# Optimization experiments

Measured on AMD Instinct MI355X. Metric: run time of the kernel, lower is better.

## Reference

```python
import jax, jax.numpy as jnp
import numpy as np

NUM_USERS = 1_000_000
NUM_AGES = 8
NUM_ATTR = 40
FACE_K = 64
VISUAL_DIM = 2048
HIDDEN = 512
BATCH = 16384
VOCAB = NUM_USERS + 24 + 2 + NUM_AGES + NUM_ATTR  # fm_linear input width


def setup_inputs() -> dict:
    key = jax.random.key(0)
    ks = jax.random.split(key, 24)
    s = 0.02
    inp = {
        "user_id": jax.random.randint(ks[0], (BATCH,), 0, NUM_USERS),
        "hour": jax.random.randint(ks[1], (BATCH,), 0, 24),
        "visual": jax.random.normal(ks[2], (BATCH, VISUAL_DIM), jnp.float32),
        "scale": jax.random.uniform(ks[3], (BATCH, 1), jnp.float32),
        "gender": jax.random.randint(ks[4], (BATCH,), 0, 2),
        "age": jax.random.randint(ks[5], (BATCH,), 0, NUM_AGES),
        "attribute": jax.random.randint(ks[6], (BATCH,), 0, NUM_ATTR),
        # embedding tables
        "user_emb": jax.random.normal(ks[7], (NUM_USERS, FACE_K), jnp.float32) * s,
        "hour_emb": jax.random.normal(ks[8], (24, FACE_K), jnp.float32) * s,
        "gender_emb": jax.random.normal(ks[9], (2, FACE_K), jnp.float32) * s,
        "age_emb": jax.random.normal(ks[10], (NUM_AGES, FACE_K), jnp.float32) * s,
        "attr_emb": jax.random.normal(ks[11], (NUM_ATTR, FACE_K), jnp.float32) * s,
        # visual linear
        "visu_w": jax.random.normal(ks[12], (FACE_K, VISUAL_DIM), jnp.float32) * s,
        "visu_b": jnp.zeros((FACE_K,), jnp.float32),
        # fm linear over concatenated one-hots (width VOCAB, out 2)
        "fm_w": jax.random.normal(ks[13], (2, VOCAB), jnp.float32) * s,
        "fm_b": jnp.zeros((2,), jnp.float32),
        # dnn
        "w1": jax.random.normal(ks[14], (HIDDEN, 6 * FACE_K), jnp.float32) * s,
        "b1": jnp.zeros((HIDDEN,), jnp.float32),
        "w2": jax.random.normal(ks[15], (HIDDEN, HIDDEN), jnp.float32) * s,
        "b2": jnp.zeros((HIDDEN,), jnp.float32),
        "w3": jax.random.normal(ks[16], (2, HIDDEN), jnp.float32) * s,
        "b3": jnp.zeros((2,), jnp.float32),
    }
    return inp


def reference(user_id, hour, visual, scale, gender, age, attribute,
              user_emb, hour_emb, gender_emb, age_emb, attr_emb,
              visu_w, visu_b, fm_w, fm_b, w1, b1, w2, b2, w3, b3):
    B = user_id.shape[0]
    # fm linear: one_hot @ W^T == gather-sum of W columns at the hot indices
    cols = jnp.stack([
        user_id,
        NUM_USERS + hour,
        NUM_USERS + 24 + gender,
        NUM_USERS + 24 + 2 + age,
        NUM_USERS + 24 + 2 + NUM_AGES + attribute,
    ], axis=1)  # [B, 5]
    linear_part = fm_w[:, cols].sum(axis=2).T + fm_b  # [B, 2]

    # embeddings
    user = user_emb[user_id]            # [B, K]
    hr = hour_emb[hour]                 # [B, K]
    face = jnp.stack([gender_emb[gender], attr_emb[attribute], age_emb[age]], axis=1)  # [B,3,K]
    face = scale[:, None, :] * jnp.tanh(face)  # scale [B,1] -> [B,1,1]
    embeddings = jnp.concatenate([user[:, None, :], hr[:, None, :], face], axis=1)  # [B,5,K]

    # FM second order
    so = jnp.square(embeddings.sum(axis=1)) - jnp.square(embeddings).sum(axis=1)  # [B,K]
    second_order = 0.5 * so.sum(axis=1)  # [B]
    fm = linear_part + second_order[:, None]  # [B,2]

    # DNN
    vis = visual @ visu_w.T + visu_b  # [B,K]
    x = jnp.concatenate([embeddings.reshape(B, 5 * FACE_K), vis], axis=1)  # [B,6K]
    x = jax.nn.relu(x @ w1.T + b1)
    x = jax.nn.relu(x @ w2.T + b2)
    x = x @ w3.T + b3
    return jax.nn.softmax(fm + x, axis=1)
```

## Files before the change

### kernel.cpp

```cpp
#include <hip/hip_runtime.h>
#include <hip/hip_bf16.h>
#include <stdint.h>

#define BATCH 16384
#define FACE_K 64
#define VISUAL_DIM 2048
#define HIDDEN 512
#define NUM_USERS 1000000
#define NUM_AGES 8
#define NUM_ATTR 40
#define VOCAB (NUM_USERS + 24 + 2 + NUM_AGES + NUM_ATTR)
#define XDIM 384
#define LDS_S 516

typedef __bf16 bf16x8 __attribute__((ext_vector_type(8)));
typedef float f32x4 __attribute__((ext_vector_type(4)));

__device__ __forceinline__ uint16_t f2bf(float f) {
    union { float f; uint32_t u; } v; v.f = f;
    uint32_t r = v.u + 0x7fffu + ((v.u >> 16) & 1u);
    return (uint16_t)(r >> 16);
}
__device__ __forceinline__ float bf2f(uint16_t h) {
    union { uint32_t u; float f; } v; v.u = ((uint32_t)h) << 16;
    return v.f;
}

__global__ void cvt_all(const float* __restrict__ visu_w, const float* __restrict__ w1,
                        const float* __restrict__ w2, uint16_t* __restrict__ vwb,
                        uint16_t* __restrict__ w1b, uint16_t* __restrict__ w2b) {
    int i = blockIdx.x * blockDim.x + threadIdx.x;
    const float4* src;
    ushort4* dst;
    if (i < 32768)       { src = (const float4*)visu_w + i;        dst = (ushort4*)vwb + i; }
    else if (i < 81920)  { src = (const float4*)w1 + (i - 32768);  dst = (ushort4*)w1b + (i - 32768); }
    else                 { src = (const float4*)w2 + (i - 81920);  dst = (ushort4*)w2b + (i - 81920); }
    float4 v = *src;
    ushort4 o;
    o.x = f2bf(v.x); o.y = f2bf(v.y); o.z = f2bf(v.z); o.w = f2bf(v.w);
    *dst = o;
}

#define VIS_BLOCKS 1024
__global__ __launch_bounds__(256) void front_kernel(
        const float* __restrict__ visual, const uint16_t* __restrict__ Wb,
        const float* __restrict__ bias,
        const int* __restrict__ uid, const int* __restrict__ hour,
        const float* __restrict__ scale, const int* __restrict__ gender,
        const int* __restrict__ age, const int* __restrict__ attr,
        const float* __restrict__ user_emb, const float* __restrict__ hour_emb,
        const float* __restrict__ gender_emb, const float* __restrict__ age_emb,
        const float* __restrict__ attr_emb,
        const float* __restrict__ fm_w, const float* __restrict__ fm_b,
        uint16_t* __restrict__ x, float* __restrict__ fm) {
    __shared__ float red[3 * 64 * 17];
    int t = threadIdx.x;
    int wv = t >> 6, lane = t & 63;

    if (blockIdx.x < VIS_BLOCKS) {
        int lc = lane & 15, quad = lane >> 4;
        int m0 = blockIdx.x * 16;
        const float*    ap = visual + (size_t)(m0 + lc) * VISUAL_DIM + wv * 512 + quad * 8;
        const uint16_t* wp = Wb + (size_t)lc * VISUAL_DIM + wv * 512 + quad * 8;

        f32x4 acc[4];
        #pragma unroll
        for (int j = 0; j < 4; ++j) acc[j] = (f32x4){0.f, 0.f, 0.f, 0.f};

        #pragma unroll 4
        for (int k = 0; k < 512; k += 32) {
            float4 a0 = *(const float4*)(ap + k);
            float4 a1 = *(const float4*)(ap + k + 4);
            bf16x8 af;
            af[0] = (__bf16)a0.x; af[1] = (__bf16)a0.y; af[2] = (__bf16)a0.z; af[3] = (__bf16)a0.w;
            af[4] = (__bf16)a1.x; af[5] = (__bf16)a1.y; af[6] = (__bf16)a1.z; af[7] = (__bf16)a1.w;
            #pragma unroll
            for (int j = 0; j < 4; ++j) {
                bf16x8 bf = *(const bf16x8*)(wp + (size_t)(j * 16) * VISUAL_DIM + k);
                acc[j] = __builtin_amdgcn_mfma_f32_16x16x32_bf16(af, bf, acc[j], 0, 0, 0);
            }
        }
        if (wv) {
            int base = (wv - 1) * 1088 + lane * 17;
            #pragma unroll
            for (int j = 0; j < 4; ++j)
                #pragma unroll
                for (int r = 0; r < 4; ++r)
                    red[base + j * 4 + r] = acc[j][r];
        }
        __syncthreads();
        if (wv == 0) {
            int base = lane * 17;
            #pragma unroll
            for (int j = 0; j < 4; ++j) {
                int col = j * 16 + lc;
                float b = bias[col];
                #pragma unroll
                for (int r = 0; r < 4; ++r) {
                    float sum = acc[j][r] + red[base + j * 4 + r]
                              + red[1088 + base + j * 4 + r] + red[2176 + base + j * 4 + r];
                    int row = m0 + quad * 4 + r;
                    x[(size_t)row * XDIM + 320 + col] = f2bf(sum + b);
                }
            }
        }
    } else {
        int row = (blockIdx.x - VIS_BLOCKS) * 4 + wv;
        int u = uid[row], h = hour[row], g = gender[row], a = age[row], at = attr[row];
        float sc = scale[row];
        float eu  = user_emb[(size_t)u * 64 + lane];
        float eh  = hour_emb[h * 64 + lane];
        float eg  = sc * tanhf(gender_emb[g * 64 + lane]);
        float eat = sc * tanhf(attr_emb[at * 64 + lane]);
        float eag = sc * tanhf(age_emb[a * 64 + lane]);
        float s  = eu + eh + eg + eat + eag;
        float sq = eu*eu + eh*eh + eg*eg + eat*eat + eag*eag;
        float so = s * s - sq;
        float l0 = 0.f, l1 = 0.f;
        if (lane < 5) {
            int col = (lane == 0) ? u
                    : (lane == 1) ? (NUM_USERS + h)
                    : (lane == 2) ? (NUM_USERS + 24 + g)
                    : (lane == 3) ? (NUM_USERS + 26 + a)
                    :               (NUM_USERS + 34 + at);
            l0 = fm_w[col];
            l1 = fm_w[VOCAB + col];
        }
        for (int m = 32; m; m >>= 1) {
            so += __shfl_xor(so, m);
            l0 += __shfl_xor(l0, m);
            l1 += __shfl_xor(l1, m);
        }
        if (lane == 0) {
            fm[row * 2 + 0] = l0 + fm_b[0] + 0.5f * so;
            fm[row * 2 + 1] = l1 + fm_b[1] + 0.5f * so;
        }
        size_t xb = (size_t)row * XDIM;
        x[xb +       lane] = f2bf(eu);
        x[xb +  64 + lane] = f2bf(eh);
        x[xb + 128 + lane] = f2bf(eg);
        x[xb + 192 + lane] = f2bf(eat);
        x[xb + 256 + lane] = f2bf(eag);
    }
}

__global__ __launch_bounds__(256) void fused_dnn(
        const uint16_t* __restrict__ x, const uint16_t* __restrict__ w1b,
        const float* __restrict__ b1, const uint16_t* __restrict__ w2b,
        const float* __restrict__ b2, const float* __restrict__ w3,
        const float* __restrict__ b3, const float* __restrict__ fm,
        float* __restrict__ out) {
    __shared__ uint16_t h1s[32 * LDS_S];
    __shared__ float dred[2][16][2];
    int t = threadIdx.x;
    int wv = t >> 6, lane = t & 63;
    int rg = wv >> 1, cs = wv & 1;
    int lc = lane & 15, quad = lane >> 4;
    int m0 = blockIdx.x * 32 + rg * 16;

    const uint16_t* ap  = x + (size_t)(m0 + lc) * XDIM + quad * 8;
    const uint16_t* wp1 = w1b + (size_t)(cs * 256 + lc) * XDIM + quad * 8;

    f32x4 acc[16];
    #pragma unroll
    for (int j = 0; j < 16; ++j) acc[j] = (f32x4){0.f, 0.f, 0.f, 0.f};

    #pragma unroll 2
    for (int ks = 0; ks < 12; ++ks) {
        bf16x8 af = *(const bf16x8*)(ap + ks * 32);
        #pragma unroll
        for (int j = 0; j < 16; ++j) {
            bf16x8 bf = *(const bf16x8*)(wp1 + (size_t)(j * 16) * XDIM + ks * 32);
            acc[j] = __builtin_amdgcn_mfma_f32_16x16x32_bf16(af, bf, acc[j], 0, 0, 0);
        }
    }
    #pragma unroll
    for (int j = 0; j < 16; ++j) {
        int col = cs * 256 + j * 16 + lc;
        float bb = b1[col];
        #pragma unroll
        for (int r = 0; r < 4; ++r) {
            float v = fmaxf(acc[j][r] + bb, 0.f);
            h1s[(rg * 16 + quad * 4 + r) * LDS_S + col] = f2bf(v);
        }
    }
    __syncthreads();

    const uint16_t* lp  = h1s + (rg * 16 + lc) * LDS_S + quad * 8;
    const uint16_t* wp2 = w2b + (size_t)(cs * 256 + lc) * HIDDEN + quad * 8;

    f32x4 acc2[16];
    #pragma unroll
    for (int j = 0; j < 16; ++j) acc2[j] = (f32x4){0.f, 0.f, 0.f, 0.f};

    #pragma unroll 2
    for (int ks = 0; ks < 16; ++ks) {
        union { bf16x8 v; ushort4 h[2]; } u;
        u.h[0] = *(const ushort4*)(lp + ks * 32);
        u.h[1] = *(const ushort4*)(lp + ks * 32 + 4);
        bf16x8 af = u.v;
        #pragma unroll
        for (int j = 0; j < 16; ++j) {
            bf16x8 bf = *(const bf16x8*)(wp2 + (size_t)(j * 16) * HIDDEN + ks * 32);
            acc2[j] = __builtin_amdgcn_mfma_f32_16x16x32_bf16(af, bf, acc2[j], 0, 0, 0);
        }
    }

    float d0[4] = {0.f, 0.f, 0.f, 0.f}, d1[4] = {0.f, 0.f, 0.f, 0.f};
    #pragma unroll
    for (int j = 0; j < 16; ++j) {
        int col = cs * 256 + j * 16 + lc;
        float bb = b2[col];
        float wa = w3[col], wb2v = w3[HIDDEN + col];
        #pragma unroll
        for (int r = 0; r < 4; ++r) {
            float v = fmaxf(acc2[j][r] + bb, 0.f);
            d0[r] += v * wa;
            d1[r] += v * wb2v;
        }
    }
    #pragma unroll
    for (int m = 1; m <= 8; m <<= 1) {
        #pragma unroll
        for (int r = 0; r < 4; ++r) {
            d0[r] += __shfl_xor(d0[r], m);
            d1[r] += __shfl_xor(d1[r], m);
        }
    }
    if (cs == 1 && lc == 0) {
        #pragma unroll
        for (int r = 0; r < 4; ++r) {
            dred[rg][quad * 4 + r][0] = d0[r];
            dred[rg][quad * 4 + r][1] = d1[r];
        }
    }
    __syncthreads();
    if (cs == 0 && lc == 0) {
        #pragma unroll
        for (int r = 0; r < 4; ++r) {
            int row = m0 + quad * 4 + r;
            float l0 = fm[row * 2 + 0] + d0[r] + dred[rg][quad * 4 + r][0] + b3[0];
            float l1 = fm[row * 2 + 1] + d1[r] + dred[rg][quad * 4 + r][1] + b3[1];
            float mx = fmaxf(l0, l1);
            float e0 = __expf(l0 - mx), e1 = __expf(l1 - mx);
            float inv = 1.f / (e0 + e1);
            out[row * 2 + 0] = e0 * inv;
            out[row * 2 + 1] = e1 * inv;
        }
    }
}

extern "C" void kernel_launch(void* const* d_in, const int* in_sizes, int n_in,
                              void* d_out, int out_size, void* d_ws, size_t ws_size,
                              hipStream_t stream) {
    const int*   user_id   = (const int*)d_in[0];
    const int*   hour      = (const int*)d_in[1];
    const float* visual    = (const float*)d_in[2];
    const float* scale     = (const float*)d_in[3];
    const int*   gender    = (const int*)d_in[4];
    const int*   age       = (const int*)d_in[5];
    const int*   attribute = (const int*)d_in[6];
    const float* user_emb  = (const float*)d_in[7];
    const float* hour_emb  = (const float*)d_in[8];
    const float* gender_emb= (const float*)d_in[9];
    const float* age_emb   = (const float*)d_in[10];
    const float* attr_emb  = (const float*)d_in[11];
    const float* visu_w    = (const float*)d_in[12];
    const float* visu_b    = (const float*)d_in[13];
    const float* fm_w      = (const float*)d_in[14];
    const float* fm_b      = (const float*)d_in[15];
    const float* w1        = (const float*)d_in[16];
    const float* b1        = (const float*)d_in[17];
    const float* w2        = (const float*)d_in[18];
    const float* b2        = (const float*)d_in[19];
    const float* w3        = (const float*)d_in[20];
    const float* b3        = (const float*)d_in[21];
    float* out = (float*)d_out;

    char* ws = (char*)d_ws;
    uint16_t* x   = (uint16_t*)ws;
    float*    fm  = (float*)   (ws + 12582912);
    uint16_t* vwb = (uint16_t*)(ws + 12582912 + 131072);
    uint16_t* w1b = vwb + 64 * 2048;
    uint16_t* w2b = w1b + 512 * 384;

    cvt_all<<<576, 256, 0, stream>>>(visu_w, w1, w2, vwb, w1b, w2b);
    front_kernel<<<VIS_BLOCKS + BATCH / 4, 256, 0, stream>>>(
        visual, vwb, visu_b,
        user_id, hour, scale, gender, age, attribute,
        user_emb, hour_emb, gender_emb, age_emb, attr_emb,
        fm_w, fm_b, x, fm);
    fused_dnn<<<BATCH / 32, 256, 0, stream>>>(x, w1b, b1, w2b, b2, w3, b3, fm, out);
}
```

Baseline: 534.1 us.

## Fuse front embedding/visual stage and DNN into one per-tile mega kernel

Merges the embedding/FM stage, the visual projection and the two-layer DNN into a single kernel where each 32-row block builds its x tile in LDS instead of writing x and fm to global memory and reading them back. The DNN GEMMs now have each wave cover 128 columns for both 16-row groups, so every weight fragment load feeds two MFMAs. This removes a kernel launch and the global round trip of the intermediate activations. In exchange the grid shrinks to 512 blocks, each running a long serial chain of phases, which lowers parallelism and latency hiding for the visual load (the dominant byte stream), and LDS use per block rises.

```diff
diff --git a/kernel.cpp b/kernel.cpp
--- a/kernel.cpp
+++ b/kernel.cpp
@@ -11,7 +11,8 @@
 #define NUM_ATTR 40
 #define VOCAB (NUM_USERS + 24 + 2 + NUM_AGES + NUM_ATTR)
 #define XDIM 384
-#define LDS_S 516
+#define XS 388
+#define HS 516
 
 typedef __bf16 bf16x8 __attribute__((ext_vector_type(8)));
 typedef float f32x4 __attribute__((ext_vector_type(4)));
@@ -20,10 +21,6 @@
     union { float f; uint32_t u; } v; v.f = f;
     uint32_t r = v.u + 0x7fffu + ((v.u >> 16) & 1u);
     return (uint16_t)(r >> 16);
-}
-__device__ __forceinline__ float bf2f(uint16_t h) {
-    union { uint32_t u; float f; } v; v.u = ((uint32_t)h) << 16;
-    return v.f;
 }
 
 __global__ void cvt_all(const float* __restrict__ visu_w, const float* __restrict__ w1,
@@ -41,211 +38,240 @@
     *dst = o;
 }
 
-#define VIS_BLOCKS 1024
-__global__ __launch_bounds__(256) void front_kernel(
-        const float* __restrict__ visual, const uint16_t* __restrict__ Wb,
-        const float* __restrict__ bias,
+__global__ __launch_bounds__(256) void mega_kernel(
         const int* __restrict__ uid, const int* __restrict__ hour,
-        const float* __restrict__ scale, const int* __restrict__ gender,
-        const int* __restrict__ age, const int* __restrict__ attr,
+        const float* __restrict__ visual, const float* __restrict__ scale,
+        const int* __restrict__ gender, const int* __restrict__ age,
+        const int* __restrict__ attr,
         const float* __restrict__ user_emb, const float* __restrict__ hour_emb,
         const float* __restrict__ gender_emb, const float* __restrict__ age_emb,
         const float* __restrict__ attr_emb,
+        const uint16_t* __restrict__ vwb, const float* __restrict__ visu_b,
         const float* __restrict__ fm_w, const float* __restrict__ fm_b,
-        uint16_t* __restrict__ x, float* __restrict__ fm) {
-    __shared__ float red[3 * 64 * 17];
+        const uint16_t* __restrict__ w1b, const float* __restrict__ b1,
+        const uint16_t* __restrict__ w2b, const float* __restrict__ b2,
+        const float* __restrict__ w3, const float* __restrict__ b3,
+        float* __restrict__ out) {
+    __shared__ uint16_t x_tile[32 * XS];
+    __shared__ uint16_t h1s[32 * HS];
+    __shared__ float red[2][16 * 64];
+    __shared__ float fm_s[32][2];
+    __shared__ float dred[4][32][2];
+
     int t = threadIdx.x;
     int wv = t >> 6, lane = t & 63;
-
-    if (blockIdx.x < VIS_BLOCKS) {
-        int lc = lane & 15, quad = lane >> 4;
-        int m0 = blockIdx.x * 16;
-        const float*    ap = visual + (size_t)(m0 + lc) * VISUAL_DIM + wv * 512 + quad * 8;
-        const uint16_t* wp = Wb + (size_t)lc * VISUAL_DIM + wv * 512 + quad * 8;
+    int lc = lane & 15, quad = lane >> 4;
+    int m0 = blockIdx.x * 32;
+
+    {
+        #pragma unroll 2
+        for (int r8 = 0; r8 < 8; ++r8) {
+            int row_l = wv * 8 + r8;
+            int row_g = m0 + row_l;
+            int u = uid[row_g], h = hour[row_g], g = gender[row_g];
+            int a = age[row_g], at = attr[row_g];
+            float sc = scale[row_g];
+            float eu  = user_emb[(size_t)u * 64 + lane];
+            float eh  = hour_emb[h * 64 + lane];
+            float eg  = sc * tanhf(gender_emb[g * 64 + lane]);
+            float eat = sc * tanhf(attr_emb[at * 64 + lane]);
+            float eag = sc * tanhf(age_emb[a * 64 + lane]);
+            float s  = eu + eh + eg + eat + eag;
+            float sq = eu*eu + eh*eh + eg*eg + eat*eat + eag*eag;
+            float so = s * s - sq;
+            float l0 = 0.f, l1 = 0.f;
+            if (lane < 5) {
+                int col = (lane == 0) ? u
+                        : (lane == 1) ? (NUM_USERS + h)
+                        : (lane == 2) ? (NUM_USERS + 24 + g)
+                        : (lane == 3) ? (NUM_USERS + 26 + a)
+                        :               (NUM_USERS + 34 + at);
+                l0 = fm_w[col];
+                l1 = fm_w[VOCAB + col];
+            }
+            for (int m = 32; m; m >>= 1) {
+                so += __shfl_xor(so, m);
+                l0 += __shfl_xor(l0, m);
+                l1 += __shfl_xor(l1, m);
+            }
+            if (lane == 0) {
+                fm_s[row_l][0] = l0 + fm_b[0] + 0.5f * so;
+                fm_s[row_l][1] = l1 + fm_b[1] + 0.5f * so;
+            }
+            int xb = row_l * XS;
+            x_tile[xb +       lane] = f2bf(eu);
+            x_tile[xb +  64 + lane] = f2bf(eh);
+            x_tile[xb + 128 + lane] = f2bf(eg);
+            x_tile[xb + 192 + lane] = f2bf(eat);
+            x_tile[xb + 256 + lane] = f2bf(eag);
+        }
+    }
+
+    {
+        int rg = wv >> 1, kh = wv & 1;
+        const float*    va = visual + (size_t)(m0 + rg * 16 + lc) * VISUAL_DIM + kh * 1024 + quad * 8;
+        const uint16_t* vb = vwb + (size_t)lc * VISUAL_DIM + kh * 1024 + quad * 8;
 
         f32x4 acc[4];
         #pragma unroll
         for (int j = 0; j < 4; ++j) acc[j] = (f32x4){0.f, 0.f, 0.f, 0.f};
 
         #pragma unroll 4
-        for (int k = 0; k < 512; k += 32) {
-            float4 a0 = *(const float4*)(ap + k);
-            float4 a1 = *(const float4*)(ap + k + 4);
+        for (int k = 0; k < 1024; k += 32) {
+            float4 a0 = *(const float4*)(va + k);
+            float4 a1 = *(const float4*)(va + k + 4);
             bf16x8 af;
             af[0] = (__bf16)a0.x; af[1] = (__bf16)a0.y; af[2] = (__bf16)a0.z; af[3] = (__bf16)a0.w;
             af[4] = (__bf16)a1.x; af[5] = (__bf16)a1.y; af[6] = (__bf16)a1.z; af[7] = (__bf16)a1.w;
             #pragma unroll
             for (int j = 0; j < 4; ++j) {
-                bf16x8 bf = *(const bf16x8*)(wp + (size_t)(j * 16) * VISUAL_DIM + k);
+                bf16x8 bf = *(const bf16x8*)(vb + (size_t)(j * 16) * VISUAL_DIM + k);
                 acc[j] = __builtin_amdgcn_mfma_f32_16x16x32_bf16(af, bf, acc[j], 0, 0, 0);
             }
         }
-        if (wv) {
-            int base = (wv - 1) * 1088 + lane * 17;
+        if (kh == 1) {
             #pragma unroll
             for (int j = 0; j < 4; ++j)
                 #pragma unroll
                 for (int r = 0; r < 4; ++r)
-                    red[base + j * 4 + r] = acc[j][r];
+                    red[rg][(quad * 4 + r) * 64 + j * 16 + lc] = acc[j][r];
         }
         __syncthreads();
-        if (wv == 0) {
-            int base = lane * 17;
+        if (kh == 0) {
             #pragma unroll
             for (int j = 0; j < 4; ++j) {
                 int col = j * 16 + lc;
-                float b = bias[col];
-                #pragma unroll
-                for (int r = 0; r < 4; ++r) {
-                    float sum = acc[j][r] + red[base + j * 4 + r]
-                              + red[1088 + base + j * 4 + r] + red[2176 + base + j * 4 + r];
-                    int row = m0 + quad * 4 + r;
-                    x[(size_t)row * XDIM + 320 + col] = f2bf(sum + b);
-                }
-            }
-        }
-    } else {
-        int row = (blockIdx.x - VIS_BLOCKS) * 4 + wv;
-        int u = uid[row], h = hour[row], g = gender[row], a = age[row], at = attr[row];
-        float sc = scale[row];
-        float eu  = user_emb[(size_t)u * 64 + lane];
-        float eh  = hour_emb[h * 64 + lane];
-        float eg  = sc * tanhf(gender_emb[g * 64 + lane]);
-        float eat = sc * tanhf(attr_emb[at * 64 + lane]);
-        float eag = sc * tanhf(age_emb[a * 64 + lane]);
-        float s  = eu + eh + eg + eat + eag;
-        float sq = eu*eu + eh*eh + eg*eg + eat*eat + eag*eag;
-        float so = s * s - sq;
-        float l0 = 0.f, l1 = 0.f;
-        if (lane < 5) {
-            int col = (lane == 0) ? u
-                    : (lane == 1) ? (NUM_USERS + h)
-                    : (lane == 2) ? (NUM_USERS + 24 + g)
-                    : (lane == 3) ? (NUM_USERS + 26 + a)
-                    :               (NUM_USERS + 34 + at);
-            l0 = fm_w[col];
-            l1 = fm_w[VOCAB + col];
-        }
-        for (int m = 32; m; m >>= 1) {
-            so += __shfl_xor(so, m);
-            l0 += __shfl_xor(l0, m);
-            l1 += __shfl_xor(l1, m);
-        }
-        if (lane == 0) {
-            fm[row * 2 + 0] = l0 + fm_b[0] + 0.5f * so;
-            fm[row * 2 + 1] = l1 + fm_b[1] + 0.5f * so;
-        }
-        size_t xb = (size_t)row * XDIM;
-        x[xb +       lane] = f2bf(eu);
-        x[xb +  64 + lane] = f2bf(eh);
-        x[xb + 128 + lane] = f2bf(eg);
-        x[xb + 192 + lane] = f2bf(eat);
-        x[xb + 256 + lane] = f2bf(eag);
-    }
-}
-
-__global__ __launch_bounds__(256) void fused_dnn(
-        const uint16_t* __restrict__ x, const uint16_t* __restrict__ w1b,
-        const float* __restrict__ b1, const uint16_t* __restrict__ w2b,
-        const float* __restrict__ b2, const float* __restrict__ w3,
-        const float* __restrict__ b3, const float* __restrict__ fm,
-        float* __restrict__ out) {
-    __shared__ uint16_t h1s[32 * LDS_S];
-    __shared__ float dred[2][16][2];
-    int t = threadIdx.x;
-    int wv = t >> 6, lane = t & 63;
-    int rg = wv >> 1, cs = wv & 1;
-    int lc = lane & 15, quad = lane >> 4;
-    int m0 = blockIdx.x * 32 + rg * 16;
-
-    const uint16_t* ap  = x + (size_t)(m0 + lc) * XDIM + quad * 8;
-    const uint16_t* wp1 = w1b + (size_t)(cs * 256 + lc) * XDIM + quad * 8;
-
-    f32x4 acc[16];
-    #pragma unroll
-    for (int j = 0; j < 16; ++j) acc[j] = (f32x4){0.f, 0.f, 0.f, 0.f};
-
-    #pragma unroll 2
-    for (int ks = 0; ks < 12; ++ks) {
-        bf16x8 af = *(const bf16x8*)(ap + ks * 32);
-        #pragma unroll
-        for (int j = 0; j < 16; ++j) {
-            bf16x8 bf = *(const bf16x8*)(wp1 + (size_t)(j * 16) * XDIM + ks * 32);
-            acc[j] = __builtin_amdgcn_mfma_f32_16x16x32_bf16(af, bf, acc[j], 0, 0, 0);
-        }
-    }
-    #pragma unroll
-    for (int j = 0; j < 16; ++j) {
-        int col = cs * 256 + j * 16 + lc;
-        float bb = b1[col];
-        #pragma unroll
-        for (int r = 0; r < 4; ++r) {
-            float v = fmaxf(acc[j][r] + bb, 0.f);
-            h1s[(rg * 16 + quad * 4 + r) * LDS_S + col] = f2bf(v);
+                float b = visu_b[col];
+                #pragma unroll
+                for (int r = 0; r < 4; ++r) {
+                    float sum = acc[j][r] + red[rg][(quad * 4 + r) * 64 + col] + b;
+                    x_tile[(rg * 16 + quad * 4 + r) * XS + 320 + col] = f2bf(sum);
+                }
+            }
         }
     }
     __syncthreads();
 
-    const uint16_t* lp  = h1s + (rg * 16 + lc) * LDS_S + quad * 8;
-    const uint16_t* wp2 = w2b + (size_t)(cs * 256 + lc) * HIDDEN + quad * 8;
-
-    f32x4 acc2[16];
-    #pragma unroll
-    for (int j = 0; j < 16; ++j) acc2[j] = (f32x4){0.f, 0.f, 0.f, 0.f};
-
-    #pragma unroll 2
-    for (int ks = 0; ks < 16; ++ks) {
-        union { bf16x8 v; ushort4 h[2]; } u;
-        u.h[0] = *(const ushort4*)(lp + ks * 32);
-        u.h[1] = *(const ushort4*)(lp + ks * 32 + 4);
-        bf16x8 af = u.v;
-        #pragma unroll
-        for (int j = 0; j < 16; ++j) {
-            bf16x8 bf = *(const bf16x8*)(wp2 + (size_t)(j * 16) * HIDDEN + ks * 32);
-            acc2[j] = __builtin_amdgcn_mfma_f32_16x16x32_bf16(af, bf, acc2[j], 0, 0, 0);
-        }
-    }
-
-    float d0[4] = {0.f, 0.f, 0.f, 0.f}, d1[4] = {0.f, 0.f, 0.f, 0.f};
-    #pragma unroll
-    for (int j = 0; j < 16; ++j) {
-        int col = cs * 256 + j * 16 + lc;
-        float bb = b2[col];
-        float wa = w3[col], wb2v = w3[HIDDEN + col];
-        #pragma unroll
-        for (int r = 0; r < 4; ++r) {
-            float v = fmaxf(acc2[j][r] + bb, 0.f);
-            d0[r] += v * wa;
-            d1[r] += v * wb2v;
-        }
-    }
-    #pragma unroll
-    for (int m = 1; m <= 8; m <<= 1) {
-        #pragma unroll
-        for (int r = 0; r < 4; ++r) {
-            d0[r] += __shfl_xor(d0[r], m);
-            d1[r] += __shfl_xor(d1[r], m);
-        }
-    }
-    if (cs == 1 && lc == 0) {
-        #pragma unroll
-        for (int r = 0; r < 4; ++r) {
-            dred[rg][quad * 4 + r][0] = d0[r];
-            dred[rg][quad * 4 + r][1] = d1[r];
+    {
+        int cs = wv;
+        const uint16_t* wp1 = w1b + (size_t)(cs * 128 + lc) * XDIM + quad * 8;
+        const uint16_t* lp0 = x_tile + lc * XS + quad * 8;
+        const uint16_t* lp1 = x_tile + (16 + lc) * XS + quad * 8;
+
+        f32x4 acc[2][8];
+        #pragma unroll
+        for (int i = 0; i < 2; ++i)
+            #pragma unroll
+            for (int j = 0; j < 8; ++j) acc[i][j] = (f32x4){0.f, 0.f, 0.f, 0.f};
+
+        #pragma unroll 2
+        for (int ks = 0; ks < 12; ++ks) {
+            union { bf16x8 v; ushort4 h[2]; } u0, u1;
+            u0.h[0] = *(const ushort4*)(lp0 + ks * 32);
+            u0.h[1] = *(const ushort4*)(lp0 + ks * 32 + 4);
+            u1.h[0] = *(const ushort4*)(lp1 + ks * 32);
+            u1.h[1] = *(const ushort4*)(lp1 + ks * 32 + 4);
+            #pragma unroll
+            for (int j = 0; j < 8; ++j) {
+                bf16x8 bf = *(const bf16x8*)(wp1 + (size_t)(j * 16) * XDIM + ks * 32);
+                acc[0][j] = __builtin_amdgcn_mfma_f32_16x16x32_bf16(u0.v, bf, acc[0][j], 0, 0, 0);
+                acc[1][j] = __builtin_amdgcn_mfma_f32_16x16x32_bf16(u1.v, bf, acc[1][j], 0, 0, 0);
+            }
+        }
+        #pragma unroll
+        for (int j = 0; j < 8; ++j) {
+            int col = cs * 128 + j * 16 + lc;
+            float bb = b1[col];
+            #pragma unroll
+            for (int i = 0; i < 2; ++i)
+                #pragma unroll
+                for (int r = 0; r < 4; ++r) {
+                    float v = fmaxf(acc[i][j][r] + bb, 0.f);
+                    h1s[(i * 16 + quad * 4 + r) * HS + col] = f2bf(v);
+                }
         }
     }
     __syncthreads();
-    if (cs == 0 && lc == 0) {
-        #pragma unroll
-        for (int r = 0; r < 4; ++r) {
-            int row = m0 + quad * 4 + r;
-            float l0 = fm[row * 2 + 0] + d0[r] + dred[rg][quad * 4 + r][0] + b3[0];
-            float l1 = fm[row * 2 + 1] + d1[r] + dred[rg][quad * 4 + r][1] + b3[1];
-            float mx = fmaxf(l0, l1);
-            float e0 = __expf(l0 - mx), e1 = __expf(l1 - mx);
-            float inv = 1.f / (e0 + e1);
-            out[row * 2 + 0] = e0 * inv;
-            out[row * 2 + 1] = e1 * inv;
+
+    {
+        int cs = wv;
+        const uint16_t* wp2 = w2b + (size_t)(cs * 128 + lc) * HIDDEN + quad * 8;
+        const uint16_t* lp0 = h1s + lc * HS + quad * 8;
+        const uint16_t* lp1 = h1s + (16 + lc) * HS + quad * 8;
+
+        f32x4 acc[2][8];
+        #pragma unroll
+        for (int i = 0; i < 2; ++i)
+            #pragma unroll
+            for (int j = 0; j < 8; ++j) acc[i][j] = (f32x4){0.f, 0.f, 0.f, 0.f};
+
+        #pragma unroll 2
+        for (int ks = 0; ks < 16; ++ks) {
+            union { bf16x8 v; ushort4 h[2]; } u0, u1;
+            u0.h[0] = *(const ushort4*)(lp0 + ks * 32);
+            u0.h[1] = *(const ushort4*)(lp0 + ks * 32 + 4);
+            u1.h[0] = *(const ushort4*)(lp1 + ks * 32);
+            u1.h[1] = *(const ushort4*)(lp1 + ks * 32 + 4);
+            #pragma unroll
+            for (int j = 0; j < 8; ++j) {
+                bf16x8 bf = *(const bf16x8*)(wp2 + (size_t)(j * 16) * HIDDEN + ks * 32);
+                acc[0][j] = __builtin_amdgcn_mfma_f32_16x16x32_bf16(u0.v, bf, acc[0][j], 0, 0, 0);
+                acc[1][j] = __builtin_amdgcn_mfma_f32_16x16x32_bf16(u1.v, bf, acc[1][j], 0, 0, 0);
+            }
+        }
+        float d0[2][4] = {{0,0,0,0},{0,0,0,0}}, d1[2][4] = {{0,0,0,0},{0,0,0,0}};
+        #pragma unroll
+        for (int j = 0; j < 8; ++j) {
+            int col = cs * 128 + j * 16 + lc;
+            float bb = b2[col];
+            float wa = w3[col], wb = w3[HIDDEN + col];
+            #pragma unroll
+            for (int i = 0; i < 2; ++i)
+                #pragma unroll
+                for (int r = 0; r < 4; ++r) {
+                    float v = fmaxf(acc[i][j][r] + bb, 0.f);
+                    d0[i][r] += v * wa;
+                    d1[i][r] += v * wb;
+                }
+        }
+        #pragma unroll
+        for (int m = 1; m <= 8; m <<= 1) {
+            #pragma unroll
+            for (int i = 0; i < 2; ++i)
+                #pragma unroll
+                for (int r = 0; r < 4; ++r) {
+                    d0[i][r] += __shfl_xor(d0[i][r], m);
+                    d1[i][r] += __shfl_xor(d1[i][r], m);
+                }
+        }
+        if (lc == 0) {
+            #pragma unroll
+            for (int i = 0; i < 2; ++i)
+                #pragma unroll
+                for (int r = 0; r < 4; ++r) {
+                    dred[cs][i * 16 + quad * 4 + r][0] = d0[i][r];
+                    dred[cs][i * 16 + quad * 4 + r][1] = d1[i][r];
+                }
+        }
+        __syncthreads();
+        if (wv == 0 && lc == 0) {
+            #pragma unroll
+            for (int i = 0; i < 2; ++i)
+                #pragma unroll
+                for (int r = 0; r < 4; ++r) {
+                    int row_l = i * 16 + quad * 4 + r;
+                    float l0 = fm_s[row_l][0] + b3[0];
+                    float l1 = fm_s[row_l][1] + b3[1];
+                    #pragma unroll
+                    for (int c = 0; c < 4; ++c) {
+                        l0 += dred[c][row_l][0];
+                        l1 += dred[c][row_l][1];
+                    }
+                    float mx = fmaxf(l0, l1);
+                    float e0 = __expf(l0 - mx), e1 = __expf(l1 - mx);
+                    float inv = 1.f / (e0 + e1);
+                    *(float2*)(out + (size_t)(m0 + row_l) * 2) = (float2){e0 * inv, e1 * inv};
+                }
         }
     }
 }
@@ -278,17 +304,13 @@
     float* out = (float*)d_out;
 
     char* ws = (char*)d_ws;
-    uint16_t* x   = (uint16_t*)ws;
-    float*    fm  = (float*)   (ws + 12582912);
-    uint16_t* vwb = (uint16_t*)(ws + 12582912 + 131072);
+    uint16_t* vwb = (uint16_t*)ws;
     uint16_t* w1b = vwb + 64 * 2048;
     uint16_t* w2b = w1b + 512 * 384;
 
     cvt_all<<<576, 256, 0, stream>>>(visu_w, w1, w2, vwb, w1b, w2b);
-    front_kernel<<<VIS_BLOCKS + BATCH / 4, 256, 0, stream>>>(
-        visual, vwb, visu_b,
-        user_id, hour, scale, gender, age, attribute,
+    mega_kernel<<<BATCH / 32, 256, 0, stream>>>(
+        user_id, hour, visual, scale, gender, age, attribute,
         user_emb, hour_emb, gender_emb, age_emb, attr_emb,
-        fm_w, fm_b, x, fm);
-    fused_dnn<<<BATCH / 32, 256, 0, stream>>>(x, w1b, b1, w2b, b2, w3, b3, fm, out);
+        vwb, visu_b, fm_w, fm_b, w1b, b1, w2b, b2, w3, b3, out);
 }
```

Result: faster. 487.5 us (-8.7%).
